# Optimization experiments

Hardware: AMD Instinct MI355X
Metric: run time of the kernel (lower is better)

Reference implementation:

```python
import jax, jax.numpy as jnp
import numpy as np
import math

B, N, D, H = 4, 2048, 1024, 16
HD = D // H  # head dim = 64


def setup_inputs() -> dict:
    key = jax.random.key(0)
    ks = jax.random.split(key, 5)
    x = jax.random.normal(ks[0], (B, N, D), dtype=jnp.float32)
    # per-head kqv Linear: weight (3*HD, D), bias (3*HD), stacked over heads
    Wkqv = jax.random.normal(ks[1], (H, 3 * HD, D), dtype=jnp.float32) / math.sqrt(D)
    bkqv = jax.random.normal(ks[2], (H, 3 * HD), dtype=jnp.float32) * 0.02
    # output projection Linear(D, D)
    Wproj = jax.random.normal(ks[3], (D, D), dtype=jnp.float32) / math.sqrt(D)
    bproj = jax.random.normal(ks[4], (D,), dtype=jnp.float32) * 0.02
    return {"x": x, "Wkqv": Wkqv, "bkqv": bkqv, "Wproj": Wproj, "bproj": bproj}


def reference(x, Wkqv, bkqv, Wproj, bproj):
    # per-head linear: y = x @ W.T + b  -> [B, H, N, 3*HD]
    kqv = jnp.einsum('bnd,hed->bhne', x, Wkqv) + bkqv[None, :, None, :]
    k, q, v = jnp.split(kqv, 3, axis=-1)  # each [B, H, N, HD]
    # scores = q @ k^T / sqrt(HD)   (attention_scores(k, q) -> q @ k.T)
    scores = jnp.einsum('bhqd,bhkd->bhqk', q, k) / math.sqrt(HD)
    causal = jnp.tril(jnp.ones((N, N), dtype=bool))
    scores = jnp.where(causal[None, None], scores, -jnp.inf)
    att = jax.nn.softmax(scores, axis=-1)
    out = jnp.einsum('bhqk,bhkd->bhqd', att, v)  # [B, H, N, HD]
    # concat heads: [B, N, H*HD]
    sa = out.transpose(0, 2, 1, 3).reshape(B, N, D)
    # dropout is identity in eval mode; final projection
    return sa @ Wproj.T + bproj
```

## Files before the change

### kernel.cpp

```cpp
#include <hip/hip_runtime.h>
#include <hip/hip_bf16.h>


#define NSEQ 2048
#define NHEAD 16
#define DMODEL 1024
#define SCALE2 0.18033688011112042f

typedef __attribute__((ext_vector_type(8))) short v8s;
typedef __attribute__((ext_vector_type(4))) float v4f;

__device__ __forceinline__ float bf2f(unsigned short u) {
    union { unsigned int i; float f; } v;
    v.i = ((unsigned int)u) << 16;
    return v.f;
}
__device__ __forceinline__ unsigned short f2bf(float f) {
    unsigned int x = __float_as_uint(f);
    return (unsigned short)((x + 0x7fffu + ((x >> 16) & 1u)) >> 16);
}
__device__ __forceinline__ unsigned short f2bf_rh(float f) {
    return (unsigned short)((__float_as_uint(f) + 0x8000u) >> 16);
}
__device__ __forceinline__ float fast_exp2(float x) {
#if __has_builtin(__builtin_amdgcn_exp2f)
    return __builtin_amdgcn_exp2f(x);
#else
    return __expf(x * 0.69314718056f);
#endif
}
__device__ __forceinline__ void gld_lds16(const unsigned short* g, unsigned short* l) {
    __builtin_amdgcn_global_load_lds(
        (const __attribute__((address_space(1))) void*)g,
        (__attribute__((address_space(3))) void*)l, 16, 0, 0);
}

__global__ __launch_bounds__(256) void cvt_bf16(
    const float* __restrict__ x, const float* __restrict__ wk, const float* __restrict__ wp,
    unsigned short* __restrict__ xb, unsigned short* __restrict__ wkb,
    unsigned short* __restrict__ wpb)
{
    const int i = blockIdx.x * 256 + threadIdx.x;
    const float* s; unsigned short* d; int o;
    if (i < 2097152)      { s = x;  d = xb;  o = i; }
    else if (i < 2883584) {
        s = wk; d = wkb;
        const int oi  = i - 2097152;
        const int row = oi >> 8, cq = oi & 255;
        const int h   = row / 192;
        const int rem = row - h * 192;
        const int cls = rem >> 6, e = rem & 63;
        float4 f = ((const float4*)s)[oi];
        ushort4 u;
        u.x = f2bf(f.x); u.y = f2bf(f.y); u.z = f2bf(f.z); u.w = f2bf(f.w);
        ((ushort4*)d)[(((cls << 10) + (h << 6) + e) << 8) + cq] = u;
        return;
    }
    else                  { s = wp; d = wpb; o = i - 2883584; }
    float4 f = ((const float4*)s)[o];
    ushort4 u;
    u.x = f2bf(f.x); u.y = f2bf(f.y); u.z = f2bf(f.z); u.w = f2bf(f.w);
    ((ushort4*)d)[o] = u;
}

template <int EPI>
__global__ __launch_bounds__(512, 4) void gemm_lds(
    const unsigned short* __restrict__ A, const unsigned short* __restrict__ B,
    const float* __restrict__ bias,
    float* __restrict__ Cf,
    unsigned short* __restrict__ Kb, unsigned short* __restrict__ Qb,
    unsigned short* __restrict__ VTb,
    int M, int Nc, int K)
{
    __shared__ __align__(16) unsigned short Al[3][4096];
    __shared__ __align__(16) unsigned short Bl[3][8192];

    const int t = threadIdx.x, wave = t >> 6, lane = t & 63;
    const int wm = wave >> 2, wn = wave & 3;

    const int lin = blockIdx.y * gridDim.x + blockIdx.x;
    const int xcd = lin & 7, pos = lin >> 3;
    const int by  = (xcd << 3) + (pos & 7);
    const int bx  = pos >> 3;
    const int m0 = by * 128, n0 = bx * 256;
    const int quad = lane >> 4, c = lane & 15;

    const int r15 = lane & 15, kg = (lane >> 4) & 3;
    const int g0 = wave * 2, g1 = wave * 2 + 1;
    const unsigned short* sA  = A + (size_t)(m0 + wave * 16 + r15) * K + kg * 8;
    const unsigned short* sB0 = B + (size_t)(n0 + g0 * 16 + r15) * K + kg * 8;
    const unsigned short* sB1 = B + (size_t)(n0 + g1 * 16 + r15) * K + kg * 8;

    v4f acc[4][4];
#pragma unroll
    for (int i = 0; i < 4; ++i)
#pragma unroll
        for (int j = 0; j < 4; ++j) acc[i][j] = (v4f){0.f, 0.f, 0.f, 0.f};

    const int fbase = (quad * 16 + c) * 8;
    const int nt = K >> 5;

    auto stage = [&](int sl, int tt) {
        const int o = tt << 5;
        gld_lds16(sA  + o, &Al[sl][wave * 512]);
        gld_lds16(sB0 + o, &Bl[sl][g0 * 512]);
        gld_lds16(sB1 + o, &Bl[sl][g1 * 512]);
    };

    stage(0, 0);
    stage(1, 1);
    asm volatile("s_waitcnt vmcnt(3)" ::: "memory");
    __builtin_amdgcn_s_barrier();

    int sl = 0;
    for (int tt = 0; tt < nt; ++tt) {
        const int sl2 = (sl == 0) ? 2 : sl - 1;
        const bool pf = (tt + 2 < nt);

        v8s af[4], bfr[4];
#pragma unroll
        for (int ms = 0; ms < 4; ++ms)
            af[ms] = *(const v8s*)&Al[sl][(wm * 4 + ms) * 512 + fbase];
#pragma unroll
        for (int ns = 0; ns < 4; ++ns)
            bfr[ns] = *(const v8s*)&Bl[sl][(wn * 4 + ns) * 512 + fbase];
        if (pf) stage(sl2, tt + 2);

        __builtin_amdgcn_s_setprio(1);
#pragma unroll
        for (int ms = 0; ms < 4; ++ms)
#pragma unroll
            for (int ns = 0; ns < 4; ++ns)
                acc[ms][ns] = __builtin_amdgcn_mfma_f32_16x16x32_bf16(
                    af[ms], bfr[ns], acc[ms][ns], 0, 0, 0);
        __builtin_amdgcn_s_setprio(0);

        if (pf) { asm volatile("s_waitcnt vmcnt(3)" ::: "memory"); }
        else    { asm volatile("s_waitcnt vmcnt(0)" ::: "memory"); }
        __builtin_amdgcn_s_barrier();
        sl = (sl == 2) ? 0 : sl + 1;
    }

#pragma unroll
    for (int ms = 0; ms < 4; ++ms) {
        const int row0 = m0 + wm * 64 + ms * 16 + quad * 4;
#pragma unroll
        for (int ns = 0; ns < 4; ++ns) {
            const int colbase = n0 + wn * 64 + ns * 16;
            float bn, scl = 1.f;
            if (EPI == 2) {
                bn = bias[colbase + c];
            } else {
                const int cls = colbase >> 10;
                const int wi  = colbase & 1023;
                const int h   = wi >> 6, e0 = wi & 63;
                bn = bias[h * 192 + cls * 64 + e0 + c];
                if (cls == 1) scl = SCALE2;
            }
            float v0 = (acc[ms][ns][0] + bn) * scl;
            float v1 = (acc[ms][ns][1] + bn) * scl;
            float v2 = (acc[ms][ns][2] + bn) * scl;
            float v3 = (acc[ms][ns][3] + bn) * scl;
            if (EPI == 2) {
                float* pc = Cf + (size_t)row0 * Nc + colbase + c;
                pc[0] = v0; pc[(size_t)Nc] = v1;
                pc[(size_t)2 * Nc] = v2; pc[(size_t)3 * Nc] = v3;
            } else {
                const int cls = colbase >> 10;
                const int wi  = colbase & 1023;
                const int h   = wi >> 6, e = (wi & 63) + c;
                const int bb  = row0 >> 11, tok0 = row0 & 2047;
                const int bhh = bb * 16 + h;
                if (cls == 2) {
                    ushort4 pk;
                    pk.x = f2bf(v0); pk.y = f2bf(v1); pk.z = f2bf(v2); pk.w = f2bf(v3);
                    *(ushort4*)(VTb + ((size_t)bhh * 64 + e) * 2048 + tok0) = pk;
                } else {
                    unsigned short* dst = (cls == 0) ? Kb : Qb;
                    const size_t base = ((size_t)bhh * 2048 + tok0) * 64 + e;
                    dst[base]       = f2bf(v0);
                    dst[base + 64]  = f2bf(v1);
                    dst[base + 128] = f2bf(v2);
                    dst[base + 192] = f2bf(v3);
                }
            }
        }
    }
}

template <int EPI>
__global__ __launch_bounds__(256, 3) void gemm128(
    const unsigned short* __restrict__ A, const unsigned short* __restrict__ B,
    const float* __restrict__ bias,
    float* __restrict__ Cf,
    int M, int Nc, int K)
{
    __shared__ __align__(16) unsigned short Al[3][4096];
    __shared__ __align__(16) unsigned short Bl[3][4096];

    const int t = threadIdx.x, wave = t >> 6, lane = t & 63;
    const int wm = wave >> 1, wn = wave & 1;

    const int lin = blockIdx.y * gridDim.x + blockIdx.x;
    const int xcd = lin & 7, pos = lin >> 3;
    const int by  = (xcd << 3) + (pos & 7);
    const int bx  = pos >> 3;
    const int m0 = by * 128, n0 = bx * 128;
    const int quad = lane >> 4, c = lane & 15;

    const int g0 = wave * 2, g1 = wave * 2 + 1;
    const int r15 = lane & 15, kg = (lane >> 4) & 3;
    const unsigned short* sA0 = A + (size_t)(m0 + g0 * 16 + r15) * K + kg * 8;
    const unsigned short* sA1 = A + (size_t)(m0 + g1 * 16 + r15) * K + kg * 8;
    const unsigned short* sB0 = B + (size_t)(n0 + g0 * 16 + r15) * K + kg * 8;
    const unsigned short* sB1 = B + (size_t)(n0 + g1 * 16 + r15) * K + kg * 8;

    v4f acc[4][4];
#pragma unroll
    for (int i = 0; i < 4; ++i)
#pragma unroll
        for (int j = 0; j < 4; ++j) acc[i][j] = (v4f){0.f, 0.f, 0.f, 0.f};

    const int fbase = (quad * 16 + c) * 8;
    const int nt = K >> 5;

    auto stage = [&](int b, int tt) {
        const int o = tt << 5;
        gld_lds16(sA0 + o, &Al[b][g0 * 512]);
        gld_lds16(sA1 + o, &Al[b][g1 * 512]);
        gld_lds16(sB0 + o, &Bl[b][g0 * 512]);
        gld_lds16(sB1 + o, &Bl[b][g1 * 512]);
    };

    stage(0, 0);
    stage(1, 1);
    asm volatile("s_waitcnt vmcnt(4)" ::: "memory");
    __builtin_amdgcn_s_barrier();

    int cur = 0;
    for (int tt = 0; tt < nt; ++tt) {
        const int nxt = (cur == 2) ? 0 : cur + 1;
        const int b2  = (nxt == 2) ? 0 : nxt + 1;
        const bool pf = (tt + 2 < nt);
        if (pf) stage(b2, tt + 2);

        v8s af[4], bfr[4];
#pragma unroll
        for (int ms = 0; ms < 4; ++ms)
            af[ms] = *(const v8s*)&Al[cur][(wm * 4 + ms) * 512 + fbase];
#pragma unroll
        for (int ns = 0; ns < 4; ++ns)
            bfr[ns] = *(const v8s*)&Bl[cur][(wn * 4 + ns) * 512 + fbase];

        __builtin_amdgcn_s_setprio(1);
#pragma unroll
        for (int ms = 0; ms < 4; ++ms)
#pragma unroll
            for (int ns = 0; ns < 4; ++ns)
                acc[ms][ns] = __builtin_amdgcn_mfma_f32_16x16x32_bf16(
                    af[ms], bfr[ns], acc[ms][ns], 0, 0, 0);
        __builtin_amdgcn_s_setprio(0);

        if (pf) { asm volatile("s_waitcnt vmcnt(4)" ::: "memory"); }
        else    { asm volatile("s_waitcnt vmcnt(0)" ::: "memory"); }
        __builtin_amdgcn_s_barrier();
        cur = nxt;
    }

#pragma unroll
    for (int ms = 0; ms < 4; ++ms) {
        const int row0 = m0 + wm * 64 + ms * 16 + quad * 4;
#pragma unroll
        for (int ns = 0; ns < 4; ++ns) {
            const int colbase = n0 + wn * 64 + ns * 16;
            const float bn = bias[colbase + c];
            float* pc = Cf + (size_t)row0 * Nc + colbase + c;
            pc[0]              = acc[ms][ns][0] + bn;
            pc[(size_t)Nc]     = acc[ms][ns][1] + bn;
            pc[(size_t)2 * Nc] = acc[ms][ns][2] + bn;
            pc[(size_t)3 * Nc] = acc[ms][ns][3] + bn;
        }
    }
}

template <bool A_BF16, int EPI>
__global__ __launch_bounds__(256) void gemm_mfma(
    const void* __restrict__ Av, const float* __restrict__ B,
    const float* __restrict__ bias,
    float* __restrict__ Cf,
    unsigned short* __restrict__ Kb, unsigned short* __restrict__ Qb,
    unsigned short* __restrict__ VTb,
    int M, int Nc, int K)
{
    __shared__ __align__(16) unsigned short Al[512 * 8];
    __shared__ __align__(16) unsigned short Bl[512 * 8];

    const int t = threadIdx.x;
    const int wave = t >> 6, lane = t & 63;
    const int wm = wave >> 1, wn = wave & 1;
    const int m0 = blockIdx.y * 128, n0 = blockIdx.x * 128;
    const int quad = lane >> 4, c = lane & 15;

    const int srow = t >> 1, skh = t & 1;
    const int sslot = (srow >> 4) * 64 + (skh * 2) * 16 + (srow & 15);

    v4f acc[4][4];
#pragma unroll
    for (int i = 0; i < 4; ++i)
#pragma unroll
        for (int j = 0; j < 4; ++j) acc[i][j] = (v4f){0.f, 0.f, 0.f, 0.f};

    const unsigned short* pa_u = (const unsigned short*)Av + (size_t)(m0 + srow) * K + skh * 16;
    const float*          pa_f = (const float*)Av          + (size_t)(m0 + srow) * K + skh * 16;
    const float*          pb   = B                          + (size_t)(n0 + srow) * K + skh * 16;

    const int fbase = (quad * 16 + c) * 8;

    for (int k0 = 0; k0 < K; k0 += 32) {
        unsigned short a16[16], b16[16];
        if (A_BF16) {
            uint4 r0 = *(const uint4*)(pa_u + k0);
            uint4 r1 = *(const uint4*)(pa_u + k0 + 8);
            *(uint4*)&a16[0] = r0; *(uint4*)&a16[8] = r1;
        } else {
            float4 f0 = *(const float4*)(pa_f + k0);
            float4 f1 = *(const float4*)(pa_f + k0 + 4);
            float4 f2 = *(const float4*)(pa_f + k0 + 8);
            float4 f3 = *(const float4*)(pa_f + k0 + 12);
            a16[0] = f2bf_rh(f0.x); a16[1] = f2bf_rh(f0.y); a16[2] = f2bf_rh(f0.z); a16[3] = f2bf_rh(f0.w);
            a16[4] = f2bf_rh(f1.x); a16[5] = f2bf_rh(f1.y); a16[6] = f2bf_rh(f1.z); a16[7] = f2bf_rh(f1.w);
            a16[8] = f2bf_rh(f2.x); a16[9] = f2bf_rh(f2.y); a16[10] = f2bf_rh(f2.z); a16[11] = f2bf_rh(f2.w);
            a16[12] = f2bf_rh(f3.x); a16[13] = f2bf_rh(f3.y); a16[14] = f2bf_rh(f3.z); a16[15] = f2bf_rh(f3.w);
        }
        {
            float4 g0 = *(const float4*)(pb + k0);
            float4 g1 = *(const float4*)(pb + k0 + 4);
            float4 g2 = *(const float4*)(pb + k0 + 8);
            float4 g3 = *(const float4*)(pb + k0 + 12);
            b16[0] = f2bf_rh(g0.x); b16[1] = f2bf_rh(g0.y); b16[2] = f2bf_rh(g0.z); b16[3] = f2bf_rh(g0.w);
            b16[4] = f2bf_rh(g1.x); b16[5] = f2bf_rh(g1.y); b16[6] = f2bf_rh(g1.z); b16[7] = f2bf_rh(g1.w);
            b16[8] = f2bf_rh(g2.x); b16[9] = f2bf_rh(g2.y); b16[10] = f2bf_rh(g2.z); b16[11] = f2bf_rh(g2.w);
            b16[12] = f2bf_rh(g3.x); b16[13] = f2bf_rh(g3.y); b16[14] = f2bf_rh(g3.z); b16[15] = f2bf_rh(g3.w);
        }
        __syncthreads();
        *(uint4*)&Al[sslot * 8]        = *(uint4*)&a16[0];
        *(uint4*)&Al[(sslot + 16) * 8] = *(uint4*)&a16[8];
        *(uint4*)&Bl[sslot * 8]        = *(uint4*)&b16[0];
        *(uint4*)&Bl[(sslot + 16) * 8] = *(uint4*)&b16[8];
        __syncthreads();

        v8s af[4], bf[4];
#pragma unroll
        for (int ms = 0; ms < 4; ++ms)
            af[ms] = *(const v8s*)&Al[(wm * 4 + ms) * 512 + fbase];
#pragma unroll
        for (int ns = 0; ns < 4; ++ns)
            bf[ns] = *(const v8s*)&Bl[(wn * 4 + ns) * 512 + fbase];
#pragma unroll
        for (int ms = 0; ms < 4; ++ms)
#pragma unroll
            for (int ns = 0; ns < 4; ++ns)
                acc[ms][ns] = __builtin_amdgcn_mfma_f32_16x16x32_bf16(
                    af[ms], bf[ns], acc[ms][ns], 0, 0, 0);
    }

#pragma unroll
    for (int ms = 0; ms < 4; ++ms) {
        const int row0 = m0 + wm * 64 + ms * 16 + quad * 4;
#pragma unroll
        for (int ns = 0; ns < 4; ++ns) {
            const int colbase = n0 + wn * 64 + ns * 16;
            float bn = (EPI == 2) ? bias[colbase + c] : bias[colbase + c];
            float v0 = acc[ms][ns][0] + bn;
            float v1 = acc[ms][ns][1] + bn;
            float v2 = acc[ms][ns][2] + bn;
            float v3 = acc[ms][ns][3] + bn;
            if (EPI == 2) {
                float* pc = Cf + (size_t)row0 * Nc + colbase + c;
                pc[0] = v0; pc[(size_t)Nc] = v1;
                pc[(size_t)2 * Nc] = v2; pc[(size_t)3 * Nc] = v3;
            } else {
                const int hh = colbase / 192;
                const int eb = colbase - hh * 192;
                const int bb = row0 >> 11, tok0 = row0 & 2047;
                const int bhh = bb * 16 + hh;
                if (eb >= 128) {
                    ushort4 pk;
                    pk.x = f2bf(v0); pk.y = f2bf(v1); pk.z = f2bf(v2); pk.w = f2bf(v3);
                    *(ushort4*)(VTb + ((size_t)bhh * 64 + (eb - 128) + c) * 2048 + tok0) = pk;
                } else {
                    const bool isq = (eb >= 64);
                    const float s = isq ? SCALE2 : 1.f;
                    unsigned short* dst = isq ? Qb : Kb;
                    const int e = (isq ? eb - 64 : eb) + c;
                    const size_t base = ((size_t)bhh * 2048 + tok0) * 64 + e;
                    dst[base]       = f2bf(v0 * s);
                    dst[base + 64]  = f2bf(v1 * s);
                    dst[base + 128] = f2bf(v2 * s);
                    dst[base + 192] = f2bf(v3 * s);
                }
            }
        }
    }
}

#define ATTS 72

__global__ __launch_bounds__(256, 2) void attn_mfma(
    const unsigned short* __restrict__ Kbuf,
    const unsigned short* __restrict__ Qbuf,
    const unsigned short* __restrict__ VT,
    unsigned short* __restrict__ sa)
{
    __shared__ __align__(16) unsigned short Ps[4][64 * ATTS];
    __shared__ __align__(16) float Mrg[2][64][81];

    const int t = threadIdx.x, w = t >> 6, lane = t & 63;
    const int quad = lane >> 4, c = lane & 15;
    const int bh = blockIdx.x & 63, bq = blockIdx.x >> 6;
    const int b = bh >> 4, hh = bh & 15;
    const size_t gbase = (size_t)bh * (2048 * 64);

    const int rs  = c & 3;
    const int rc0 = (quad ^ rs) * 8, rc1 = 32 + rc0;
    unsigned short* PsW = &Ps[w][0];

    const int qtA = (w == 0) ? bq : (w == 1) ? (15 - bq) : (w == 2) ? (16 + bq) : (31 - bq);
    const int kA1 = (w == 0) ? (bq + 1) : (w == 1) ? (16 - bq) : 17;
    const int qtB = (w == 0) ? (31 - bq) : (16 + bq);
    const int kB1 = (w == 0) ? (32 - bq) : (17 + bq);

    v4f oacc[4][4], lacc[4];
    const short oneb = (short)0x3F80;
    const v8s ones = {oneb, oneb, oneb, oneb, oneb, oneb, oneb, oneb};

    auto run_seg = [&](int qt, int k0, int k1) {
        const int qw = qt * 64;
        v8s qf[4][2];
#pragma unroll
        for (int qs = 0; qs < 4; ++qs) {
            const unsigned short* qp =
                Qbuf + gbase + (size_t)(qw + qs * 16 + c) * 64 + quad * 8;
            qf[qs][0] = *(const v8s*)qp;
            qf[qs][1] = *(const v8s*)(qp + 32);
        }
#pragma unroll
        for (int qs = 0; qs < 4; ++qs) {
            lacc[qs] = (v4f){0.f, 0.f, 0.f, 0.f};
#pragma unroll
            for (int dn = 0; dn < 4; ++dn) oacc[qs][dn] = (v4f){0.f, 0.f, 0.f, 0.f};
        }
        for (int kt = k0; kt < k1; ++kt) {
            const int kbase = kt * 64;
            const bool diag = (kt == qt);

            v8s vf[4][2];
#pragma unroll
            for (int dn = 0; dn < 4; ++dn) {
                const unsigned short* vp =
                    VT + gbase + (size_t)(dn * 16 + c) * 2048 + kbase + quad * 8;
                vf[dn][0] = *(const v8s*)vp;
                vf[dn][1] = *(const v8s*)(vp + 32);
            }

#pragma unroll
            for (int kn = 0; kn < 4; ++kn) {
                const unsigned short* kp =
                    Kbuf + gbase + (size_t)(kbase + kn * 16 + c) * 64 + quad * 8;
                v8s kf0 = *(const v8s*)kp;
                v8s kf1 = *(const v8s*)(kp + 32);
#pragma unroll
                for (int qs = 0; qs < 4; ++qs) {
                    v4f s = (v4f){0.f, 0.f, 0.f, 0.f};
                    s = __builtin_amdgcn_mfma_f32_16x16x32_bf16(qf[qs][0], kf0, s, 0, 0, 0);
                    s = __builtin_amdgcn_mfma_f32_16x16x32_bf16(qf[qs][1], kf1, s, 0, 0, 0);
                    if (diag) {
#pragma unroll
                        for (int r = 0; r < 4; ++r)
                            if (kn * 16 + c > qs * 16 + quad * 4 + r) s[r] = -1e30f;
                    }
#pragma unroll
                    for (int r = 0; r < 4; ++r) {
                        const float p = fast_exp2(s[r]);
                        PsW[(qs * 16 + quad * 4 + r) * ATTS +
                            (((2 * kn + (c >> 3)) ^ r) * 8) + (c & 7)] = f2bf_rh(p);
                    }
                }
            }
            v8s pa[4][2];
#pragma unroll
            for (int qs = 0; qs < 4; ++qs) {
                pa[qs][0] = *(const v8s*)&PsW[(qs * 16 + c) * ATTS + rc0];
                pa[qs][1] = *(const v8s*)&PsW[(qs * 16 + c) * ATTS + rc1];
            }
#pragma unroll
            for (int dn = 0; dn < 4; ++dn) {
#pragma unroll
                for (int qs = 0; qs < 4; ++qs) {
                    oacc[qs][dn] = __builtin_amdgcn_mfma_f32_16x16x32_bf16(pa[qs][0], vf[dn][0], oacc[qs][dn], 0, 0, 0);
                    oacc[qs][dn] = __builtin_amdgcn_mfma_f32_16x16x32_bf16(pa[qs][1], vf[dn][1], oacc[qs][dn], 0, 0, 0);
                }
            }
#pragma unroll
            for (int qs = 0; qs < 4; ++qs) {
                lacc[qs] = __builtin_amdgcn_mfma_f32_16x16x32_bf16(pa[qs][0], ones, lacc[qs], 0, 0, 0);
                lacc[qs] = __builtin_amdgcn_mfma_f32_16x16x32_bf16(pa[qs][1], ones, lacc[qs], 0, 0, 0);
            }
        }
    };

    auto store_final = [&](int qt) {
        const int qw = qt * 64;
#pragma unroll
        for (int qs = 0; qs < 4; ++qs) {
            float inv[4];
#pragma unroll
            for (int r = 0; r < 4; ++r) inv[r] = 1.f / lacc[qs][r];
            const size_t obase =
                ((size_t)(b * 2048 + qw + qs * 16 + quad * 4)) * DMODEL + hh * 64;
#pragma unroll
            for (int dn = 0; dn < 4; ++dn)
#pragma unroll
                for (int r = 0; r < 4; ++r)
                    sa[obase + (size_t)r * DMODEL + dn * 16 + c] = f2bf(oacc[qs][dn][r] * inv[r]);
        }
    };

    run_seg(qtA, 0, kA1);
    if (w < 2) {
        store_final(qtA);
        run_seg(qtB, 17, kB1);
        float* mg = &Mrg[w][lane][0];
#pragma unroll
        for (int qs = 0; qs < 4; ++qs) {
#pragma unroll
            for (int dn = 0; dn < 4; ++dn)
#pragma unroll
                for (int r = 0; r < 4; ++r) mg[qs * 16 + dn * 4 + r] = oacc[qs][dn][r];
#pragma unroll
            for (int r = 0; r < 4; ++r) mg[64 + qs * 4 + r] = lacc[qs][r];
        }
    }
    __syncthreads();
    if (w >= 2) {
        const float* mg = &Mrg[3 - w][lane][0];
#pragma unroll
        for (int qs = 0; qs < 4; ++qs) {
#pragma unroll
            for (int dn = 0; dn < 4; ++dn)
#pragma unroll
                for (int r = 0; r < 4; ++r) oacc[qs][dn][r] += mg[qs * 16 + dn * 4 + r];
#pragma unroll
            for (int r = 0; r < 4; ++r) lacc[qs][r] += mg[64 + qs * 4 + r];
        }
        store_final(qtA);
    }
}

extern "C" void kernel_launch(void* const* d_in, const int* in_sizes, int n_in,
                              void* d_out, int out_size, void* d_ws, size_t ws_size,
                              hipStream_t stream) {
    const float* x     = (const float*)d_in[0];
    const float* Wkqv  = (const float*)d_in[1];
    const float* bkqv  = (const float*)d_in[2];
    const float* Wproj = (const float*)d_in[3];
    const float* bproj = (const float*)d_in[4];
    float* out = (float*)d_out;

    unsigned short* Kb = (unsigned short*)d_ws;
    unsigned short* Qb = Kb + (size_t)8388608;
    unsigned short* VT = Qb + (size_t)8388608;
    unsigned short* sa = VT + (size_t)8388608;

    const bool fast = ws_size >= 75497472ull;
    if (fast) {
        unsigned short* xb  = sa;
        unsigned short* wkb = (unsigned short*)d_ws + (size_t)33554432;
        unsigned short* wpb = wkb + (size_t)3145728;
        cvt_bf16<<<12288, 256, 0, stream>>>(x, Wkqv, Wproj, xb, wkb, wpb);
        gemm_lds<1><<<dim3(12, 64), 512, 0, stream>>>(
            xb, wkb, bkqv, nullptr, Kb, Qb, VT, 8192, 3072, 1024);
        attn_mfma<<<512, 256, 0, stream>>>(Kb, Qb, VT, sa);
        gemm128<2><<<dim3(8, 64), 256, 0, stream>>>(
            sa, wpb, bproj, out, 8192, 1024, 1024);
    } else {
        gemm_mfma<false, 1><<<dim3(24, 64), 256, 0, stream>>>(
            x, Wkqv, bkqv, nullptr, Kb, Qb, VT, 8192, 3072, 1024);
        attn_mfma<<<512, 256, 0, stream>>>(Kb, Qb, VT, sa);
        gemm_mfma<true, 2><<<dim3(8, 64), 256, 0, stream>>>(
            sa, Wproj, bproj, out, nullptr, nullptr, nullptr, 8192, 1024, 1024);
    }
}
```

Before: 276.7 us.

## Fuse x fp32-to-bf16 conversion into KQV GEMM A-loading; use 256-wide tiles for projection

After: 312.7 us. 13.0% more time.

```diff
diff --git a/kernel.cpp b/kernel.cpp
--- a/kernel.cpp
+++ b/kernel.cpp
@@ -36,31 +36,157 @@
 }
 
 __global__ __launch_bounds__(256) void cvt_bf16(
-    const float* __restrict__ x, const float* __restrict__ wk, const float* __restrict__ wp,
-    unsigned short* __restrict__ xb, unsigned short* __restrict__ wkb,
-    unsigned short* __restrict__ wpb)
+    const float* __restrict__ wk, const float* __restrict__ wp,
+    unsigned short* __restrict__ wkb, unsigned short* __restrict__ wpb)
 {
     const int i = blockIdx.x * 256 + threadIdx.x;
-    const float* s; unsigned short* d; int o;
-    if (i < 2097152)      { s = x;  d = xb;  o = i; }
-    else if (i < 2883584) {
-        s = wk; d = wkb;
-        const int oi  = i - 2097152;
-        const int row = oi >> 8, cq = oi & 255;
+    if (i < 786432) {
+        const int row = i >> 8, cq = i & 255;
         const int h   = row / 192;
         const int rem = row - h * 192;
         const int cls = rem >> 6, e = rem & 63;
-        float4 f = ((const float4*)s)[oi];
+        float4 f = ((const float4*)wk)[i];
         ushort4 u;
         u.x = f2bf(f.x); u.y = f2bf(f.y); u.z = f2bf(f.z); u.w = f2bf(f.w);
-        ((ushort4*)d)[(((cls << 10) + (h << 6) + e) << 8) + cq] = u;
-        return;
-    }
-    else                  { s = wp; d = wpb; o = i - 2883584; }
-    float4 f = ((const float4*)s)[o];
-    ushort4 u;
-    u.x = f2bf(f.x); u.y = f2bf(f.y); u.z = f2bf(f.z); u.w = f2bf(f.w);
-    ((ushort4*)d)[o] = u;
+        ((ushort4*)wkb)[(((cls << 10) + (h << 6) + e) << 8) + cq] = u;
+    } else {
+        const int o = i - 786432;
+        float4 f = ((const float4*)wp)[o];
+        ushort4 u;
+        u.x = f2bf(f.x); u.y = f2bf(f.y); u.z = f2bf(f.z); u.w = f2bf(f.w);
+        ((ushort4*)wpb)[o] = u;
+    }
+}
+
+__global__ __launch_bounds__(512, 4) void gemm_kqv(
+    const float* __restrict__ X, const unsigned short* __restrict__ B,
+    const float* __restrict__ bias,
+    unsigned short* __restrict__ Kb, unsigned short* __restrict__ Qb,
+    unsigned short* __restrict__ VTb,
+    int M, int Nc, int K)
+{
+    __shared__ __align__(16) unsigned short Al[3][4096];
+    __shared__ __align__(16) unsigned short Bl[3][8192];
+
+    const int t = threadIdx.x, wave = t >> 6, lane = t & 63;
+    const int wm = wave >> 2, wn = wave & 3;
+
+    const int lin = blockIdx.y * gridDim.x + blockIdx.x;
+    const int xcd = lin & 7, pos = lin >> 3;
+    const int by  = (xcd << 3) + (pos & 7);
+    const int bx  = pos >> 3;
+    const int m0 = by * 128, n0 = bx * 256;
+    const int quad = lane >> 4, c = lane & 15;
+
+    const int r15 = lane & 15, kg = (lane >> 4) & 3;
+    const int g0 = wave * 2, g1 = wave * 2 + 1;
+    const float* sAf = X + (size_t)(m0 + wave * 16 + r15) * K + kg * 8;
+    const unsigned short* sB0 = B + (size_t)(n0 + g0 * 16 + r15) * K + kg * 8;
+    const unsigned short* sB1 = B + (size_t)(n0 + g1 * 16 + r15) * K + kg * 8;
+
+    v4f acc[4][4];
+#pragma unroll
+    for (int i = 0; i < 4; ++i)
+#pragma unroll
+        for (int j = 0; j < 4; ++j) acc[i][j] = (v4f){0.f, 0.f, 0.f, 0.f};
+
+    const int fbase = (quad * 16 + c) * 8;
+    const int nt = K >> 5;
+
+    float4 pa0, pa1;
+    auto loadA = [&](int tt) {
+        const float* p = sAf + (size_t)tt * 32;
+        pa0 = *(const float4*)p;
+        pa1 = *(const float4*)(p + 4);
+    };
+    auto writeA = [&](int sl) {
+        unsigned short tmp[8] = {
+            f2bf(pa0.x), f2bf(pa0.y), f2bf(pa0.z), f2bf(pa0.w),
+            f2bf(pa1.x), f2bf(pa1.y), f2bf(pa1.z), f2bf(pa1.w)};
+        *(uint4*)&Al[sl][wave * 512 + lane * 8] = *(const uint4*)tmp;
+    };
+    auto stageB = [&](int sl, int tt) {
+        const int o = tt << 5;
+        gld_lds16(sB0 + o, &Bl[sl][g0 * 512]);
+        gld_lds16(sB1 + o, &Bl[sl][g1 * 512]);
+    };
+
+    loadA(0);
+    stageB(0, 0);
+    asm volatile("s_waitcnt vmcnt(0)" ::: "memory");
+    writeA(0);
+    loadA(1);
+    stageB(1, 1);
+    asm volatile("s_waitcnt lgkmcnt(0)" ::: "memory");
+    __builtin_amdgcn_s_barrier();
+
+    for (int tt = 0; tt < nt; ++tt) {
+        const int sl  = tt % 3;
+        const int sl1 = (tt + 1) % 3;
+        const int sl2 = (tt + 2) % 3;
+
+        v8s af[4], bfr[4];
+#pragma unroll
+        for (int ms = 0; ms < 4; ++ms)
+            af[ms] = *(const v8s*)&Al[sl][(wm * 4 + ms) * 512 + fbase];
+#pragma unroll
+        for (int ns = 0; ns < 4; ++ns)
+            bfr[ns] = *(const v8s*)&Bl[sl][(wn * 4 + ns) * 512 + fbase];
+
+        if (tt + 1 < nt) {
+            asm volatile("s_waitcnt vmcnt(0)" ::: "memory");
+            writeA(sl1);
+        }
+        if (tt + 2 < nt) {
+            loadA(tt + 2);
+            stageB(sl2, tt + 2);
+        }
+
+        __builtin_amdgcn_s_setprio(1);
+#pragma unroll
+        for (int ms = 0; ms < 4; ++ms)
+#pragma unroll
+            for (int ns = 0; ns < 4; ++ns)
+                acc[ms][ns] = __builtin_amdgcn_mfma_f32_16x16x32_bf16(
+                    af[ms], bfr[ns], acc[ms][ns], 0, 0, 0);
+        __builtin_amdgcn_s_setprio(0);
+
+        asm volatile("s_waitcnt lgkmcnt(0)" ::: "memory");
+        __builtin_amdgcn_s_barrier();
+    }
+
+#pragma unroll
+    for (int ms = 0; ms < 4; ++ms) {
+        const int row0 = m0 + wm * 64 + ms * 16 + quad * 4;
+#pragma unroll
+        for (int ns = 0; ns < 4; ++ns) {
+            const int colbase = n0 + wn * 64 + ns * 16;
+            const int cls = colbase >> 10;
+            const int wi  = colbase & 1023;
+            const int h   = wi >> 6, e0 = wi & 63;
+            const float bn = bias[h * 192 + cls * 64 + e0 + c];
+            const float scl = (cls == 1) ? SCALE2 : 1.f;
+            float v0 = (acc[ms][ns][0] + bn) * scl;
+            float v1 = (acc[ms][ns][1] + bn) * scl;
+            float v2 = (acc[ms][ns][2] + bn) * scl;
+            float v3 = (acc[ms][ns][3] + bn) * scl;
+            const int e   = e0 + c;
+            const int bb  = row0 >> 11, tok0 = row0 & 2047;
+            const int bhh = bb * 16 + h;
+            if (cls == 2) {
+                ushort4 pk;
+                pk.x = f2bf(v0); pk.y = f2bf(v1); pk.z = f2bf(v2); pk.w = f2bf(v3);
+                *(ushort4*)(VTb + ((size_t)bhh * 64 + e) * 2048 + tok0) = pk;
+            } else {
+                unsigned short* dst = (cls == 0) ? Kb : Qb;
+                const size_t base = ((size_t)bhh * 2048 + tok0) * 64 + e;
+                dst[base]       = f2bf(v0);
+                dst[base + 64]  = f2bf(v1);
+                dst[base + 128] = f2bf(v2);
+                dst[base + 192] = f2bf(v3);
+            }
+        }
+    }
 }
 
 template <int EPI>
@@ -139,132 +265,6 @@
         else    { asm volatile("s_waitcnt vmcnt(0)" ::: "memory"); }
         __builtin_amdgcn_s_barrier();
         sl = (sl == 2) ? 0 : sl + 1;
-    }
-
-#pragma unroll
-    for (int ms = 0; ms < 4; ++ms) {
-        const int row0 = m0 + wm * 64 + ms * 16 + quad * 4;
-#pragma unroll
-        for (int ns = 0; ns < 4; ++ns) {
-            const int colbase = n0 + wn * 64 + ns * 16;
-            float bn, scl = 1.f;
-            if (EPI == 2) {
-                bn = bias[colbase + c];
-            } else {
-                const int cls = colbase >> 10;
-                const int wi  = colbase & 1023;
-                const int h   = wi >> 6, e0 = wi & 63;
-                bn = bias[h * 192 + cls * 64 + e0 + c];
-                if (cls == 1) scl = SCALE2;
-            }
-            float v0 = (acc[ms][ns][0] + bn) * scl;
-            float v1 = (acc[ms][ns][1] + bn) * scl;
-            float v2 = (acc[ms][ns][2] + bn) * scl;
-            float v3 = (acc[ms][ns][3] + bn) * scl;
-            if (EPI == 2) {
-                float* pc = Cf + (size_t)row0 * Nc + colbase + c;
-                pc[0] = v0; pc[(size_t)Nc] = v1;
-                pc[(size_t)2 * Nc] = v2; pc[(size_t)3 * Nc] = v3;
-            } else {
-                const int cls = colbase >> 10;
-                const int wi  = colbase & 1023;
-                const int h   = wi >> 6, e = (wi & 63) + c;
-                const int bb  = row0 >> 11, tok0 = row0 & 2047;
-                const int bhh = bb * 16 + h;
-                if (cls == 2) {
-                    ushort4 pk;
-                    pk.x = f2bf(v0); pk.y = f2bf(v1); pk.z = f2bf(v2); pk.w = f2bf(v3);
-                    *(ushort4*)(VTb + ((size_t)bhh * 64 + e) * 2048 + tok0) = pk;
-                } else {
-                    unsigned short* dst = (cls == 0) ? Kb : Qb;
-                    const size_t base = ((size_t)bhh * 2048 + tok0) * 64 + e;
-                    dst[base]       = f2bf(v0);
-                    dst[base + 64]  = f2bf(v1);
-                    dst[base + 128] = f2bf(v2);
-                    dst[base + 192] = f2bf(v3);
-                }
-            }
-        }
-    }
-}
-
-template <int EPI>
-__global__ __launch_bounds__(256, 3) void gemm128(
-    const unsigned short* __restrict__ A, const unsigned short* __restrict__ B,
-    const float* __restrict__ bias,
-    float* __restrict__ Cf,
-    int M, int Nc, int K)
-{
-    __shared__ __align__(16) unsigned short Al[3][4096];
-    __shared__ __align__(16) unsigned short Bl[3][4096];
-
-    const int t = threadIdx.x, wave = t >> 6, lane = t & 63;
-    const int wm = wave >> 1, wn = wave & 1;
-
-    const int lin = blockIdx.y * gridDim.x + blockIdx.x;
-    const int xcd = lin & 7, pos = lin >> 3;
-    const int by  = (xcd << 3) + (pos & 7);
-    const int bx  = pos >> 3;
-    const int m0 = by * 128, n0 = bx * 128;
-    const int quad = lane >> 4, c = lane & 15;
-
-    const int g0 = wave * 2, g1 = wave * 2 + 1;
-    const int r15 = lane & 15, kg = (lane >> 4) & 3;
-    const unsigned short* sA0 = A + (size_t)(m0 + g0 * 16 + r15) * K + kg * 8;
-    const unsigned short* sA1 = A + (size_t)(m0 + g1 * 16 + r15) * K + kg * 8;
-    const unsigned short* sB0 = B + (size_t)(n0 + g0 * 16 + r15) * K + kg * 8;
-    const unsigned short* sB1 = B + (size_t)(n0 + g1 * 16 + r15) * K + kg * 8;
-
-    v4f acc[4][4];
-#pragma unroll
-    for (int i = 0; i < 4; ++i)
-#pragma unroll
-        for (int j = 0; j < 4; ++j) acc[i][j] = (v4f){0.f, 0.f, 0.f, 0.f};
-
-    const int fbase = (quad * 16 + c) * 8;
-    const int nt = K >> 5;
-
-    auto stage = [&](int b, int tt) {
-        const int o = tt << 5;
-        gld_lds16(sA0 + o, &Al[b][g0 * 512]);
-        gld_lds16(sA1 + o, &Al[b][g1 * 512]);
-        gld_lds16(sB0 + o, &Bl[b][g0 * 512]);
-        gld_lds16(sB1 + o, &Bl[b][g1 * 512]);
-    };
-
-    stage(0, 0);
-    stage(1, 1);
-    asm volatile("s_waitcnt vmcnt(4)" ::: "memory");
-    __builtin_amdgcn_s_barrier();
-
-    int cur = 0;
-    for (int tt = 0; tt < nt; ++tt) {
-        const int nxt = (cur == 2) ? 0 : cur + 1;
-        const int b2  = (nxt == 2) ? 0 : nxt + 1;
-        const bool pf = (tt + 2 < nt);
-        if (pf) stage(b2, tt + 2);
-
-        v8s af[4], bfr[4];
-#pragma unroll
-        for (int ms = 0; ms < 4; ++ms)
-            af[ms] = *(const v8s*)&Al[cur][(wm * 4 + ms) * 512 + fbase];
-#pragma unroll
-        for (int ns = 0; ns < 4; ++ns)
-            bfr[ns] = *(const v8s*)&Bl[cur][(wn * 4 + ns) * 512 + fbase];
-
-        __builtin_amdgcn_s_setprio(1);
-#pragma unroll
-        for (int ms = 0; ms < 4; ++ms)
-#pragma unroll
-            for (int ns = 0; ns < 4; ++ns)
-                acc[ms][ns] = __builtin_amdgcn_mfma_f32_16x16x32_bf16(
-                    af[ms], bfr[ns], acc[ms][ns], 0, 0, 0);
-        __builtin_amdgcn_s_setprio(0);
-
-        if (pf) { asm volatile("s_waitcnt vmcnt(4)" ::: "memory"); }
-        else    { asm volatile("s_waitcnt vmcnt(0)" ::: "memory"); }
-        __builtin_amdgcn_s_barrier();
-        cur = nxt;
     }
 
 #pragma unroll
@@ -574,15 +574,14 @@
 
     const bool fast = ws_size >= 75497472ull;
     if (fast) {
-        unsigned short* xb  = sa;
         unsigned short* wkb = (unsigned short*)d_ws + (size_t)33554432;
         unsigned short* wpb = wkb + (size_t)3145728;
-        cvt_bf16<<<12288, 256, 0, stream>>>(x, Wkqv, Wproj, xb, wkb, wpb);
-        gemm_lds<1><<<dim3(12, 64), 512, 0, stream>>>(
-            xb, wkb, bkqv, nullptr, Kb, Qb, VT, 8192, 3072, 1024);
+        cvt_bf16<<<4096, 256, 0, stream>>>(Wkqv, Wproj, wkb, wpb);
+        gemm_kqv<<<dim3(12, 64), 512, 0, stream>>>(
+            x, wkb, bkqv, Kb, Qb, VT, 8192, 3072, 1024);
         attn_mfma<<<512, 256, 0, stream>>>(Kb, Qb, VT, sa);
-        gemm128<2><<<dim3(8, 64), 256, 0, stream>>>(
-            sa, wpb, bproj, out, 8192, 1024, 1024);
+        gemm_lds<2><<<dim3(4, 64), 512, 0, stream>>>(
+            sa, wpb, bproj, out, nullptr, nullptr, nullptr, 8192, 1024, 1024);
     } else {
         gemm_mfma<false, 1><<<dim3(24, 64), 256, 0, stream>>>(
             x, Wkqv, bkqv, nullptr, Kb, Qb, VT, 8192, 3072, 1024);
```
